# Optimization experiments

Hardware: AMD Instinct MI355X
Metric: run time of the kernel (lower is better)

The kernel has to match this reference:

```python
import jax, jax.numpy as jnp
import numpy as np


def _norm_group(pts, ref):
    # pts: [B,T,N,2], ref: [B,T,1,2]. Subtract reference point, divide both coords
    # by max(width,height) of the relative bbox (per frame), guarding scale==0.
    rel = pts - ref
    w = rel[..., 0].max(axis=-1) - rel[..., 0].min(axis=-1)
    h = rel[..., 1].max(axis=-1) - rel[..., 1].min(axis=-1)
    s = jnp.maximum(w, h)
    s = jnp.where(s == 0, jnp.ones_like(s), s)
    return rel / s[..., None, None]


def _prepare_input(x):
    B, T, _ = x.shape
    pts = x.reshape(B, T, 133, 2)
    left = _norm_group(pts[:, :, 91:112], pts[:, :, 9:10]).reshape(B, T, 42)
    right = _norm_group(pts[:, :, 112:133], pts[:, :, 10:11]).reshape(B, T, 42)
    center = pts[:, :, 0:1]
    left_arm = _norm_group(pts[:, :, (5, 7, 9), :], center).reshape(B, T, 6)
    right_arm = _norm_group(pts[:, :, (6, 8, 10), :], center).reshape(B, T, 6)
    return right, right_arm, left, left_arm


def _lstm(x, wih, whh, bih, bhh):
    # x: [B,T,F]; PyTorch gate order i,f,g,o. Returns all hidden states [B,T,H].
    B = x.shape[0]
    H = whh.shape[1]
    pre = jnp.einsum('btf,gf->btg', x, wih) + bih  # [B,T,4H]
    pre = pre.transpose(1, 0, 2)  # time-major for scan
    h0 = jnp.zeros((B, H), x.dtype)
    c0 = jnp.zeros((B, H), x.dtype)

    def step(carry, xt):
        h, c = carry
        g = xt + h @ whh.T + bhh
        i, f, gg, o = jnp.split(g, 4, axis=-1)
        i = jax.nn.sigmoid(i)
        f = jax.nn.sigmoid(f)
        gg = jnp.tanh(gg)
        o = jax.nn.sigmoid(o)
        c = f * c + i * gg
        h = o * jnp.tanh(c)
        return (h, c), h

    _, hs = jax.lax.scan(step, (h0, c0), pre)
    return hs.transpose(1, 0, 2)


def setup_inputs() -> dict:
    key = jax.random.key(0)
    ks = jax.random.split(key, 24)
    B, T = 128, 512
    NUM_CLASSES = 250
    HID = 2 * 64 + 2 * 32  # 192
    s = 0.1

    def p(k, shape):
        return jax.random.normal(k, shape, dtype=jnp.float32) * s

    inp = {'x': jax.random.normal(ks[0], (B, T, 266), dtype=jnp.float32)}
    # right hand LSTM: 42 -> 64
    inp['wih_rh'] = p(ks[1], (256, 42)); inp['whh_rh'] = p(ks[2], (256, 64))
    inp['bih_rh'] = p(ks[3], (256,));   inp['bhh_rh'] = p(ks[4], (256,))
    # right arm LSTM: 6 -> 32
    inp['wih_ra'] = p(ks[5], (128, 6));  inp['whh_ra'] = p(ks[6], (128, 32))
    inp['bih_ra'] = p(ks[7], (128,));   inp['bhh_ra'] = p(ks[8], (128,))
    # left hand LSTM: 42 -> 64
    inp['wih_lh'] = p(ks[9], (256, 42)); inp['whh_lh'] = p(ks[10], (256, 64))
    inp['bih_lh'] = p(ks[11], (256,));  inp['bhh_lh'] = p(ks[12], (256,))
    # left arm LSTM: 6 -> 32
    inp['wih_la'] = p(ks[13], (128, 6)); inp['whh_la'] = p(ks[14], (128, 32))
    inp['bih_la'] = p(ks[15], (128,));  inp['bhh_la'] = p(ks[16], (128,))
    # attention (Linear(192,1,bias=False)) and fc
    inp['att_w'] = p(ks[17], (1, HID))
    inp['fc_w'] = p(ks[18], (NUM_CLASSES, HID))
    inp['fc_b'] = p(ks[19], (NUM_CLASSES,))
    return inp


def reference(x, wih_rh, whh_rh, bih_rh, bhh_rh,
              wih_ra, whh_ra, bih_ra, bhh_ra,
              wih_lh, whh_lh, bih_lh, bhh_lh,
              wih_la, whh_la, bih_la, bhh_la,
              att_w, fc_w, fc_b):
    rh, ra, lh, la = _prepare_input(x)
    rh_out = _lstm(rh, wih_rh, whh_rh, bih_rh, bhh_rh)
    ra_out = _lstm(ra, wih_ra, whh_ra, bih_ra, bhh_ra)
    lh_out = _lstm(lh, wih_lh, whh_lh, bih_lh, bhh_lh)
    la_out = _lstm(la, wih_la, whh_la, bih_la, bhh_la)
    combined = jnp.concatenate([rh_out, ra_out, lh_out, la_out], axis=2)  # [B,T,192]
    scores = jnp.einsum('bth,oh->bto', combined, att_w)  # [B,T,1]
    weights = jax.nn.softmax(scores, axis=1)
    context = jnp.sum(weights * combined, axis=1)  # [B,192]
    out = context @ fc_w.T + fc_b  # [B,num_classes]
    return out, weights
```

## Files before the change

kernel.cpp:

```cpp
#include <hip/hip_runtime.h>
#include <math.h>

#define BATCH 128
#define TLEN 512
#define XF 266
#define HID 192
#define NC 250

typedef __attribute__((ext_vector_type(8))) short short8;
typedef __attribute__((ext_vector_type(4))) float float4v;

#define NL2E  -1.4426950408889634f
#define NL2E2 -2.8853900817779268f

__device__ __forceinline__ unsigned short f2bf(float f) {
  unsigned u = __float_as_uint(f);
  u += 0x7FFF + ((u >> 16) & 1);
  return (unsigned short)(u >> 16);
}
__device__ __forceinline__ float bf2f(unsigned short s) {
  return __uint_as_float(((unsigned)s) << 16);
}

__device__ __forceinline__ float exp2i(float x) {
#if __has_builtin(__builtin_amdgcn_exp2f)
  return __builtin_amdgcn_exp2f(x);
#else
  float r;
  asm("v_exp_f32 %0, %1" : "=v"(r) : "v"(x));
  return r;
#endif
}

__device__ __forceinline__ void lds_barrier() {
  asm volatile("s_waitcnt lgkmcnt(0)\n\ts_barrier" ::: "memory");
}


__device__ __forceinline__ void norm_hand(const float* __restrict__ xp,
                                          unsigned short* __restrict__ fp,
                                          int p0, int refp, int hs) {
  float rx = xp[2 * refp], ry = xp[2 * refp + 1];
  float px[21], py[21];
  float minx = 1e30f, maxx = -1e30f, miny = 1e30f, maxy = -1e30f;
#pragma unroll
  for (int i = 0; i < 21; ++i) {
    float ax = xp[2 * (p0 + i)] - rx;
    float ay = xp[2 * (p0 + i) + 1] - ry;
    px[i] = ax; py[i] = ay;
    minx = fminf(minx, ax); maxx = fmaxf(maxx, ax);
    miny = fminf(miny, ay); maxy = fmaxf(maxy, ay);
  }
  float s = fmaxf(maxx - minx, maxy - miny);
  if (s == 0.f) s = 1.f;
  float inv = 1.f / s;
#pragma unroll
  for (int i = 0; i < 21; ++i) {
    fp[2 * i] = f2bf(px[i] * inv);
    fp[2 * i + 1] = f2bf(py[i] * inv);
  }
  for (int i = 42; i < hs; ++i) fp[i] = 0;
}

__device__ __forceinline__ void norm_arm(const float* __restrict__ xp,
                                         unsigned short* __restrict__ fp,
                                         int a, int b, int c) {
  float rx = xp[0], ry = xp[1];
  float x0 = xp[2 * a] - rx, y0 = xp[2 * a + 1] - ry;
  float x1 = xp[2 * b] - rx, y1 = xp[2 * b + 1] - ry;
  float x2 = xp[2 * c] - rx, y2 = xp[2 * c + 1] - ry;
  float w = fmaxf(fmaxf(x0, x1), x2) - fminf(fminf(x0, x1), x2);
  float h = fmaxf(fmaxf(y0, y1), y2) - fminf(fminf(y0, y1), y2);
  float s = fmaxf(w, h);
  if (s == 0.f) s = 1.f;
  float inv = 1.f / s;
  fp[0] = f2bf(x0 * inv); fp[1] = f2bf(y0 * inv);
  fp[2] = f2bf(x1 * inv); fp[3] = f2bf(y1 * inv);
  fp[4] = f2bf(x2 * inv); fp[5] = f2bf(y2 * inv);
  fp[6] = 0; fp[7] = 0;
}

__global__ __launch_bounds__(256) void prep_kernel(
    const float* __restrict__ x,
    unsigned short* __restrict__ fHR, unsigned short* __restrict__ fHL,
    unsigned short* __restrict__ fAR, unsigned short* __restrict__ fAL,
    int mode) {
  int idx = blockIdx.x * 256 + threadIdx.x;
  if (idx >= BATCH * TLEN) return;
  int b = idx >> 9, t = idx & 511;
  const float* xp = x + (size_t)idx * XF;
  size_t hoff, aoff;
  int hs;
  if (mode) {
    hs = 64;
    int vh = b & 7;
    int rowh = (vh >> 1) * 4 + (vh & 1);
    hoff = (((size_t)(b >> 3) * TLEN + t) * 16 + rowh) * 64;
    int va = b & 15;
    int rowa = (va >> 3) * 16 + ((va & 7) >> 1) * 4 + (va & 1);
    aoff = (((size_t)(b >> 4) * TLEN + t) * 32 + rowa) * 8;
  } else {
    hs = 48;
    hoff = (((size_t)(b >> 4) * TLEN + t) * 16 + (b & 15)) * 48;
    aoff = (((size_t)(b >> 5) * TLEN + t) * 32 + (b & 31)) * 8;
  }
  norm_hand(xp, fHR + hoff, 112, 10, hs);
  norm_hand(xp, fHL + hoff, 91, 9, hs);
  norm_arm (xp, fAR + aoff, 6, 8, 10);
  norm_arm (xp, fAL + aoff, 5, 7, 9);
}


__global__ __launch_bounds__(256) void pack_kernel(
    int mode,
    const float* __restrict__ wi_rh, const float* __restrict__ wh_rh,
    const float* __restrict__ wi_ra, const float* __restrict__ wh_ra,
    const float* __restrict__ wi_lh, const float* __restrict__ wh_lh,
    const float* __restrict__ wi_la, const float* __restrict__ wh_la,
    unsigned short* __restrict__ btA_r, unsigned short* __restrict__ btA_l,
    unsigned short* __restrict__ btH_r, unsigned short* __restrict__ btH_l,
    unsigned short* __restrict__ btArm_r, unsigned short* __restrict__ btArm_l) {
  int blk = blockIdx.x, tid = threadIdx.x;
  if (blk < 2) {
    const float* wi = blk ? wi_lh : wi_rh;
    const float* wh = blk ? wh_lh : wh_rh;
    unsigned short* dst = blk ? btA_l : btA_r;
    if (mode) {
      for (int i = tid; i < 256 * 64; i += 256) {
        int g = i >> 6, k = i & 63;
        float s = ((g >> 6) == 2) ? NL2E2 : NL2E;
        dst[i] = f2bf(k < 42 ? wi[g * 42 + k] * s : 0.f);
      }
    } else {
      for (int i = tid; i < 256 * 128; i += 256) {
        int g = i >> 7, k = i & 127;
        float s = ((g >> 6) == 2) ? NL2E2 : NL2E;
        float v = (k < 42) ? wi[g * 42 + k] : (k < 64 ? 0.f : wh[g * 64 + (k - 64)]);
        dst[i] = f2bf(v * s);
      }
    }
  } else if (blk < 4) {
    if (mode) {
      const float* wh = (blk == 3) ? wh_lh : wh_rh;
      unsigned short* dst = (blk == 3) ? btH_l : btH_r;
      for (int i = tid; i < 256 * 64; i += 256) {
        int g = i >> 6;
        float s = ((g >> 6) == 2) ? NL2E2 : NL2E;
        dst[i] = f2bf(wh[i] * s);
      }
    }
  } else {
    const float* wi = (blk == 5) ? wi_la : wi_ra;
    const float* wh = (blk == 5) ? wh_la : wh_ra;
    unsigned short* dst = (blk == 5) ? btArm_l : btArm_r;
    for (int i = tid; i < 128 * 64; i += 256) {
      int g = i >> 6, k = i & 63;
      float s = ((g >> 5) == 2) ? NL2E2 : NL2E;
      float v = (k < 6) ? wi[g * 6 + k] : (k < 32 ? 0.f : wh[g * 32 + (k - 32)]);
      dst[i] = f2bf(v * s);
    }
  }
}


__global__ __launch_bounds__(256, 1) void pregemm_kernel(
    const unsigned short* __restrict__ f64R, const unsigned short* __restrict__ f64L,
    const unsigned short* __restrict__ btiR, const unsigned short* __restrict__ btiL,
    const float* __restrict__ biR, const float* __restrict__ bhR,
    const float* __restrict__ biL, const float* __restrict__ bhL,
    unsigned short* __restrict__ preR, unsigned short* __restrict__ preL) {
  int bx = blockIdx.x;
  int lr = bx >> 8, tile = (bx >> 4) & 15, tc = bx & 15;
  const unsigned short* f64 = lr ? f64L : f64R;
  const unsigned short* bti = lr ? btiL : btiR;
  const float* bi = lr ? biL : biR;
  const float* bh = lr ? bhL : bhR;
  unsigned short* pre = lr ? preL : preR;
  int tid = threadIdx.x, lane = tid & 63;
  int q = tid >> 6, n = lane & 15, quad = lane >> 4;
  float sq = (q == 2) ? NL2E2 : NL2E;

  short8 Vb[4][2];
  float bias[4];
#pragma unroll
  for (int jg = 0; jg < 4; ++jg) {
    int g = q * 64 + jg * 16 + n;
    bias[jg] = (bi[g] + bh[g]) * sq;
#pragma unroll
    for (int c = 0; c < 2; ++c)
      Vb[jg][c] = *(const short8*)(bti + (size_t)g * 64 + c * 32 + quad * 8);
  }

  for (int i = 0; i < 32; ++i) {
    int t = tc * 32 + i;
    const unsigned short* ap = f64 + ((size_t)(tile * 512 + t) * 16 + n) * 64 + quad * 8;
    short8 Va0 = *(const short8*)ap;
    short8 Va1 = *(const short8*)(ap + 32);
    unsigned short* pb = pre + (size_t)(tile * 512 + t) * 2048 + n * 32 + quad * 8 + q * 2;
#pragma unroll
    for (int jg = 0; jg < 4; ++jg) {
      float4v acc = {bias[jg], bias[jg], bias[jg], bias[jg]};
      acc = __builtin_amdgcn_mfma_f32_16x16x32_bf16(Va0, Vb[jg][0], acc, 0, 0, 0);
      acc = __builtin_amdgcn_mfma_f32_16x16x32_bf16(Va1, Vb[jg][1], acc, 0, 0, 0);
      unsigned w = (unsigned)f2bf(acc[0]) | ((unsigned)f2bf(acc[1]) << 16);
      *(unsigned*)(pb + (size_t)jg * 512) = w;
    }
  }
}


template <int H, int CH, int STR, int MB, int SCH, int HOFF, bool HOIST, int RV>
__device__ __forceinline__ void lstm_core(
    unsigned short* __restrict__ Ab0, unsigned short* __restrict__ Ab1,
    const unsigned short* __restrict__ Bt,
    const float* __restrict__ bi, const float* __restrict__ bh,
    const unsigned short* __restrict__ featp,
    const unsigned short* __restrict__ prep_,
    unsigned short* __restrict__ combbase,
    int b0, int mrow0, int j0) {
  constexpr int K = CH * 32;
  constexpr int XSH = MB * SCH * 8;
  constexpr int JQ = H / 4;
  constexpr int VR = (RV == 4) ? MB : MB / 2;
  int tid = threadIdx.x;
  int lane = tid & 63, n = lane & 15, quad = lane >> 4;

  short8 Vb[4][CH];
  float bias[4];
#pragma unroll
  for (int q = 0; q < 4; ++q) {
    int g = q * H + j0 + n;
    if (!HOIST) bias[q] = (bi[g] + bh[g]) * ((q == 2) ? NL2E2 : NL2E);
#pragma unroll
    for (int c = 0; c < CH; ++c)
      Vb[q][c] = *(const short8*)(Bt + (size_t)g * K + c * 32 + quad * 8);
  }

  for (int i = tid; i < MB * STR; i += 256) { Ab0[i] = 0; Ab1[i] = 0; }
  __syncthreads();

  bool st = false;
  unsigned short *xd0 = nullptr, *xd1 = nullptr;
  const unsigned short* fp = nullptr;
  short8 xE, xO;
  if (!HOIST) {
    st = tid < MB * SCH;
    int sm = tid / SCH, sc8 = tid % SCH;
    xd0 = Ab0 + sm * STR + sc8 * 8;
    xd1 = Ab1 + sm * STR + sc8 * 8;
    fp = featp + tid * 8;
    if (st) {
      *(short8*)xd0 = *(const short8*)fp;
      xO = *(const short8*)(fp + XSH);
      xE = *(const short8*)(fp + 2 * (size_t)XSH);
    }
    fp += 3 * (size_t)XSH;
  }

  const unsigned short* ppE = nullptr;
  const unsigned short* ppO = nullptr;
  short8 pE, pO;
  if (HOIST) {
    const unsigned short* pp0 = prep_ + (size_t)j0 * 32 + n * 32 + quad * 8;
    pE = *(const short8*)pp0;
    pO = *(const short8*)(pp0 + 2048);
    ppE = pp0 + 2 * (size_t)2048;
    ppO = pp0 + 3 * (size_t)2048;
  }

  float4v cc = {0.f, 0.f, 0.f, 0.f};
  __syncthreads();

  const unsigned short* ard0 = Ab0 + (mrow0 + n) * STR;
  const unsigned short* ard1 = Ab1 + (mrow0 + n) * STR;
  unsigned short* hw0 = Ab0 + (mrow0 + quad * 4) * STR + HOFF + j0 + n;
  unsigned short* hw1 = Ab1 + (mrow0 + quad * 4) * STR + HOFF + j0 + n;

  int vi = tid / JQ, fjq = tid % JQ;
  bool fon = tid < VR * JQ;
  int fm = (RV == 4) ? vi
                     : ((vi >> 3) * 16 + ((vi & 7) >> 1) * 4 + (vi & 1));
  const unsigned short* fl0 = Ab0 + fm * STR + HOFF + fjq * 4;
  const unsigned short* fl1 = Ab1 + fm * STR + HOFF + fjq * 4;
  unsigned short* cfp = combbase + ((size_t)(b0 + vi) * TLEN) * HID + fjq * 4;

#define ACT_AND_WRITE(hw)                                                     \
  _Pragma("unroll")                                                           \
  for (int r = 0; r < RV; ++r) {                                              \
    float Ei = exp2i(acc[0][r]);                                              \
    float Ef = exp2i(acc[1][r]);                                              \
    float Eg = exp2i(acc[2][r]);                                              \
    float Eo = exp2i(acc[3][r]);                                              \
    float gf = __builtin_amdgcn_rcpf(1.f + Ef);                               \
    float ig = (1.f - Eg) * __builtin_amdgcn_rcpf((1.f + Ei) * (1.f + Eg));   \
    float cv = fmaf(gf, cc[r], ig);                                           \
    cc[r] = cv;                                                               \
    float Ec = exp2i(cv * NL2E2);                                             \
    float hv = (1.f - Ec) * __builtin_amdgcn_rcpf((1.f + Eo) * (1.f + Ec));   \
    (hw)[r * STR] = f2bf(hv);                                                 \
  }

  for (int tt = 0; tt < TLEN; tt += 2) {
    {
      const int t = tt;
      if (fon && t > 0) {
        *(uint2*)cfp = *(const uint2*)fl0;
        cfp += HID;
      }
      short8 Va[CH];
#pragma unroll
      for (int c = 0; c < CH; ++c)
        Va[c] = *(const short8*)(ard0 + c * 32 + quad * 8);

      float4v acc[4];
      if (HOIST) {
#pragma unroll
        for (int q = 0; q < 4; ++q) {
          acc[q][0] = bf2f((unsigned short)pE[q * 2]);
          acc[q][1] = bf2f((unsigned short)pE[q * 2 + 1]);
          acc[q][2] = 0.f; acc[q][3] = 0.f;
        }
        if (t + 2 < TLEN) pE = *(const short8*)ppE;
        ppE += 2 * (size_t)2048;
      } else {
#pragma unroll
        for (int q = 0; q < 4; ++q)
          acc[q] = (float4v){bias[q], bias[q], bias[q], bias[q]};
      }
#pragma unroll
      for (int q = 0; q < 4; ++q)
#pragma unroll
        for (int c = 0; c < CH; ++c)
          acc[q] = __builtin_amdgcn_mfma_f32_16x16x32_bf16(Va[c], Vb[q][c], acc[q], 0, 0, 0);

      if (!HOIST) {
        if (st) {
          *(short8*)xd1 = xO;
          if (t + 3 < TLEN) xO = *(const short8*)fp;
        }
        fp += XSH;
      }

      ACT_AND_WRITE(hw1)
      lds_barrier();
    }
    {
      const int t = tt + 1;
      if (fon) {
        *(uint2*)cfp = *(const uint2*)fl1;
        cfp += HID;
      }
      short8 Va[CH];
#pragma unroll
      for (int c = 0; c < CH; ++c)
        Va[c] = *(const short8*)(ard1 + c * 32 + quad * 8);

      float4v acc[4];
      if (HOIST) {
#pragma unroll
        for (int q = 0; q < 4; ++q) {
          acc[q][0] = bf2f((unsigned short)pO[q * 2]);
          acc[q][1] = bf2f((unsigned short)pO[q * 2 + 1]);
          acc[q][2] = 0.f; acc[q][3] = 0.f;
        }
        if (t + 2 < TLEN) pO = *(const short8*)ppO;
        ppO += 2 * (size_t)2048;
      } else {
#pragma unroll
        for (int q = 0; q < 4; ++q)
          acc[q] = (float4v){bias[q], bias[q], bias[q], bias[q]};
      }
#pragma unroll
      for (int q = 0; q < 4; ++q)
#pragma unroll
        for (int c = 0; c < CH; ++c)
          acc[q] = __builtin_amdgcn_mfma_f32_16x16x32_bf16(Va[c], Vb[q][c], acc[q], 0, 0, 0);

      if (!HOIST) {
        if (st) {
          if (t + 1 < TLEN) *(short8*)xd0 = xE;
          if (t + 3 < TLEN) xE = *(const short8*)fp;
        }
        fp += XSH;
      }

      ACT_AND_WRITE(hw0)
      lds_barrier();
    }
  }

  if (fon) *(uint2*)cfp = *(const uint2*)fl0;
#undef ACT_AND_WRITE
}

__global__ __launch_bounds__(256, 1) void lstm_hoist(
    const unsigned short* __restrict__ fAR, const unsigned short* __restrict__ fAL,
    const unsigned short* __restrict__ btH_r, const unsigned short* __restrict__ btH_l,
    const unsigned short* __restrict__ btArm_r, const unsigned short* __restrict__ btArm_l,
    const unsigned short* __restrict__ preR, const unsigned short* __restrict__ preL,
    const float* __restrict__ b1i, const float* __restrict__ b1h,
    const float* __restrict__ b3i, const float* __restrict__ b3h,
    unsigned short* __restrict__ combined) {
  __shared__ __align__(16) unsigned short A0[2304];
  __shared__ __align__(16) unsigned short A1[2304];
  int blk = blockIdx.x;
  int wave = threadIdx.x >> 6;
  if (blk < 32) {
    int lr = blk >> 4, tl = blk & 15;
    lstm_core<64, 2, 72, 16, 0, 0, true, 2>(
        A0, A1, lr ? btH_l : btH_r, nullptr, nullptr, nullptr,
        (lr ? preL : preR) + (size_t)tl * 512 * 2048,
        combined + (lr ? 96 : 0), tl * 8, 0, wave * 16);
  } else {
    int a = blk - 32;
    int la = a >> 3, tl = a & 7;
    lstm_core<32, 2, 72, 32, 1, 32, false, 2>(
        A0, A1, la ? btArm_l : btArm_r, la ? b3i : b1i, la ? b3h : b1h,
        (la ? fAL : fAR) + (size_t)tl * 512 * 256, nullptr,
        combined + (la ? 160 : 64), tl * 16, (wave >> 1) * 16, (wave & 1) * 16);
  }
}

__global__ __launch_bounds__(256, 1) void lstm_fb(
    const unsigned short* __restrict__ fHR, const unsigned short* __restrict__ fHL,
    const unsigned short* __restrict__ fAR, const unsigned short* __restrict__ fAL,
    const unsigned short* __restrict__ btA_r, const unsigned short* __restrict__ btA_l,
    const unsigned short* __restrict__ btArm_r, const unsigned short* __restrict__ btArm_l,
    const float* __restrict__ b0i, const float* __restrict__ b0h,
    const float* __restrict__ b1i, const float* __restrict__ b1h,
    const float* __restrict__ b2i, const float* __restrict__ b2h,
    const float* __restrict__ b3i, const float* __restrict__ b3h,
    unsigned short* __restrict__ combined) {
  __shared__ __align__(16) unsigned short A0[2304];
  __shared__ __align__(16) unsigned short A1[2304];
  int blk = blockIdx.x;
  int wave = threadIdx.x >> 6;
  if (blk < 16) {
    int lr = blk >> 3, tl = blk & 7;
    lstm_core<64, 4, 136, 16, 6, 64, false, 4>(
        A0, A1, lr ? btA_l : btA_r, lr ? b2i : b0i, lr ? b2h : b0h,
        (lr ? fHL : fHR) + (size_t)tl * 512 * 768, nullptr,
        combined + (lr ? 96 : 0), tl * 16, 0, wave * 16);
  } else {
    int a = blk - 16;
    int la = a >> 2, tl = a & 3;
    lstm_core<32, 2, 72, 32, 1, 32, false, 4>(
        A0, A1, la ? btArm_l : btArm_r, la ? b3i : b1i, la ? b3h : b1h,
        (la ? fAL : fAR) + (size_t)tl * 512 * 256, nullptr,
        combined + (la ? 160 : 64), tl * 32, (wave >> 1) * 16, (wave & 1) * 16);
  }
}


__global__ __launch_bounds__(512) void attn_kernel(const unsigned short* __restrict__ combined,
                                                   const float* __restrict__ att_w,
                                                   const float* __restrict__ fc_w,
                                                   const float* __restrict__ fc_b,
                                                   float* __restrict__ dout) {
  __shared__ float sc[TLEN];
  __shared__ float aw[HID];
  __shared__ float pctx[8][HID];
  __shared__ float ctx[HID];
  __shared__ float red[8];
  int b = blockIdx.x, tid = threadIdx.x;
  int lane = tid & 63, wave = tid >> 6;
  const unsigned short* cb = combined + (size_t)b * TLEN * HID;
  if (tid < HID) aw[tid] = att_w[tid];
  __syncthreads();
  float a0 = aw[lane], a1 = aw[lane + 64], a2 = aw[lane + 128];

  int t0 = wave * 64;
  for (int t = t0; t < t0 + 64; t += 2) {
    const unsigned short* r0 = cb + (size_t)t * HID;
    const unsigned short* r1 = r0 + HID;
    float p0 = a0 * bf2f(r0[lane]) + a1 * bf2f(r0[lane + 64]) + a2 * bf2f(r0[lane + 128]);
    float p1 = a0 * bf2f(r1[lane]) + a1 * bf2f(r1[lane + 64]) + a2 * bf2f(r1[lane + 128]);
#pragma unroll
    for (int o = 32; o; o >>= 1) {
      p0 += __shfl_xor(p0, o, 64);
      p1 += __shfl_xor(p1, o, 64);
    }
    if (lane == 0) { sc[t] = p0; sc[t + 1] = p1; }
  }
  __syncthreads();

  float e = sc[tid];
  float lmax = e;
#pragma unroll
  for (int o = 32; o; o >>= 1) lmax = fmaxf(lmax, __shfl_xor(lmax, o, 64));
  if (lane == 0) red[wave] = lmax;
  __syncthreads();
  float m = red[0];
#pragma unroll
  for (int w = 1; w < 8; ++w) m = fmaxf(m, red[w]);
  __syncthreads();
  float ex = __expf(e - m);
  float ls = ex;
#pragma unroll
  for (int o = 32; o; o >>= 1) ls += __shfl_xor(ls, o, 64);
  if (lane == 0) red[wave] = ls;
  __syncthreads();
  float S = red[0];
#pragma unroll
  for (int w = 1; w < 8; ++w) S += red[w];
  float wgt = ex / S;
  sc[tid] = wgt;
  dout[BATCH * NC + b * TLEN + tid] = wgt;
  __syncthreads();

#pragma unroll
  for (int p = 0; p < 3; ++p) {
    int h = p * 64 + lane;
    float c0 = 0.f, c1 = 0.f, c2 = 0.f, c3 = 0.f;
    for (int t = t0; t < t0 + 64; t += 4) {
      c0 += sc[t] * bf2f(cb[(size_t)t * HID + h]);
      c1 += sc[t + 1] * bf2f(cb[(size_t)(t + 1) * HID + h]);
      c2 += sc[t + 2] * bf2f(cb[(size_t)(t + 2) * HID + h]);
      c3 += sc[t + 3] * bf2f(cb[(size_t)(t + 3) * HID + h]);
    }
    pctx[wave][h] = (c0 + c1) + (c2 + c3);
  }
  __syncthreads();
  if (tid < HID) {
    float s = pctx[0][tid];
#pragma unroll
    for (int w = 1; w < 8; ++w) s += pctx[w][tid];
    ctx[tid] = s;
  }
  __syncthreads();

  if (tid < NC) {
    const float* wr = fc_w + (size_t)tid * HID;
    float s0 = fc_b[tid], s1 = 0.f, s2 = 0.f, s3 = 0.f;
#pragma unroll
    for (int h = 0; h < HID; h += 4) {
      s0 += ctx[h] * wr[h];
      s1 += ctx[h + 1] * wr[h + 1];
      s2 += ctx[h + 2] * wr[h + 2];
      s3 += ctx[h + 3] * wr[h + 3];
    }
    dout[b * NC + tid] = (s0 + s1) + (s2 + s3);
  }
}


extern "C" void kernel_launch(void* const* d_in, const int* in_sizes, int n_in,
                              void* d_out, int out_size, void* d_ws, size_t ws_size,
                              hipStream_t stream) {
  const float* x = (const float*)d_in[0];
  const float* wih_rh = (const float*)d_in[1];
  const float* whh_rh = (const float*)d_in[2];
  const float* bih_rh = (const float*)d_in[3];
  const float* bhh_rh = (const float*)d_in[4];
  const float* wih_ra = (const float*)d_in[5];
  const float* whh_ra = (const float*)d_in[6];
  const float* bih_ra = (const float*)d_in[7];
  const float* bhh_ra = (const float*)d_in[8];
  const float* wih_lh = (const float*)d_in[9];
  const float* whh_lh = (const float*)d_in[10];
  const float* bih_lh = (const float*)d_in[11];
  const float* bhh_lh = (const float*)d_in[12];
  const float* wih_la = (const float*)d_in[13];
  const float* whh_la = (const float*)d_in[14];
  const float* bih_la = (const float*)d_in[15];
  const float* bhh_la = (const float*)d_in[16];
  const float* att_w = (const float*)d_in[17];
  const float* fc_w = (const float*)d_in[18];
  const float* fc_b = (const float*)d_in[19];

  const size_t SZ_COMB   = (size_t)BATCH * TLEN * HID * 2;
  const size_t SZ_FARM_H = (size_t)8 * TLEN * 32 * 8 * 2;
  const size_t SZ_FARM_F = (size_t)4 * TLEN * 32 * 8 * 2;
  const size_t SZ_F64    = (size_t)16 * TLEN * 16 * 64 * 2;
  const size_t SZ_F48    = (size_t)8 * TLEN * 16 * 48 * 2;
  const size_t SZ_PRE    = (size_t)16 * TLEN * 2048 * 2;
  const size_t NEED_FULL = SZ_COMB + 2 * SZ_FARM_H + 2 * SZ_F64 + 2 * SZ_PRE +
                           2 * 32768 + 2 * 32768 + 2 * 16384;
  bool hoist = ws_size >= NEED_FULL;

  char* p = (char*)d_ws;
  unsigned short* combined = (unsigned short*)p; p += SZ_COMB;
  unsigned short *fAR, *fAL;
  unsigned short *fHR, *fHL, *preR = nullptr, *preL = nullptr;
  unsigned short *btA_r, *btA_l, *btH_r = nullptr, *btH_l = nullptr, *btArm_r, *btArm_l;
  if (hoist) {
    fAR = (unsigned short*)p; p += SZ_FARM_H;
    fAL = (unsigned short*)p; p += SZ_FARM_H;
    fHR = (unsigned short*)p; p += SZ_F64;
    fHL = (unsigned short*)p; p += SZ_F64;
    preR = (unsigned short*)p; p += SZ_PRE;
    preL = (unsigned short*)p; p += SZ_PRE;
    btA_r = (unsigned short*)p; p += 32768;
    btA_l = (unsigned short*)p; p += 32768;
    btH_r = (unsigned short*)p; p += 32768;
    btH_l = (unsigned short*)p; p += 32768;
  } else {
    fAR = (unsigned short*)p; p += SZ_FARM_F;
    fAL = (unsigned short*)p; p += SZ_FARM_F;
    fHR = (unsigned short*)p; p += SZ_F48;
    fHL = (unsigned short*)p; p += SZ_F48;
    btA_r = (unsigned short*)p; p += 65536;
    btA_l = (unsigned short*)p; p += 65536;
    btH_r = btA_r; btH_l = btA_l;
  }
  btArm_r = (unsigned short*)p; p += 16384;
  btArm_l = (unsigned short*)p;

  prep_kernel<<<dim3((BATCH * TLEN + 255) / 256), 256, 0, stream>>>(
      x, fHR, fHL, fAR, fAL, hoist ? 1 : 0);
  pack_kernel<<<dim3(6), 256, 0, stream>>>(
      hoist ? 1 : 0,
      wih_rh, whh_rh, wih_ra, whh_ra, wih_lh, whh_lh, wih_la, whh_la,
      btA_r, btA_l, btH_r, btH_l, btArm_r, btArm_l);
  if (hoist) {
    pregemm_kernel<<<dim3(512), 256, 0, stream>>>(
        fHR, fHL, btA_r, btA_l, bih_rh, bhh_rh, bih_lh, bhh_lh, preR, preL);
    lstm_hoist<<<dim3(48), 256, 0, stream>>>(
        fAR, fAL, btH_r, btH_l, btArm_r, btArm_l, preR, preL,
        bih_ra, bhh_ra, bih_la, bhh_la, combined);
  } else {
    lstm_fb<<<dim3(24), 256, 0, stream>>>(
        fHR, fHL, fAR, fAL, btA_r, btA_l, btArm_r, btArm_l,
        bih_rh, bhh_rh, bih_ra, bhh_ra, bih_lh, bhh_lh, bih_la, bhh_la, combined);
  }
  attn_kernel<<<dim3(BATCH), 512, 0, stream>>>(combined, att_w, fc_w, fc_b, (float*)d_out);
}
```

Before: 438.8 us.

## Restructure hoisted LSTM into single-wave blocks with 4 sequences each

Replaces the 256-thread recurrent LSTM blocks, which shared hidden state through LDS with a block barrier every timestep, with 128 single-wave blocks that each run 4 batch sequences. Each wave keeps all gate weights in registers and computes every gate tile itself, so the per-step s_barrier goes away and only an LDS wait remains. The input and pre-gate layouts are reorganized to match, and weight packing is folded into the consuming kernels, which removes the pack launch on the hoisted path. The trade-off is more MFMA work per wave and much heavier register use, across more blocks in parallel.

```diff
diff --git a/kernel.cpp b/kernel.cpp
--- a/kernel.cpp
+++ b/kernel.cpp
@@ -30,10 +30,6 @@
   asm("v_exp_f32 %0, %1" : "=v"(r) : "v"(x));
   return r;
 #endif
-}
-
-__device__ __forceinline__ void lds_barrier() {
-  asm volatile("s_waitcnt lgkmcnt(0)\n\ts_barrier" ::: "memory");
 }
 
 
@@ -93,12 +89,8 @@
   int hs;
   if (mode) {
     hs = 64;
-    int vh = b & 7;
-    int rowh = (vh >> 1) * 4 + (vh & 1);
-    hoff = (((size_t)(b >> 3) * TLEN + t) * 16 + rowh) * 64;
-    int va = b & 15;
-    int rowa = (va >> 3) * 16 + ((va & 7) >> 1) * 4 + (va & 1);
-    aoff = (((size_t)(b >> 4) * TLEN + t) * 32 + rowa) * 8;
+    hoff = (((size_t)(b >> 4) * TLEN + t) * 16 + (b & 15)) * 64;
+    aoff = (((size_t)(b >> 2) * TLEN + t) * 4 + (b & 3)) * 8;
   } else {
     hs = 48;
     hoff = (((size_t)(b >> 4) * TLEN + t) * 16 + (b & 15)) * 48;
@@ -112,47 +104,27 @@
 
 
 __global__ __launch_bounds__(256) void pack_kernel(
-    int mode,
     const float* __restrict__ wi_rh, const float* __restrict__ wh_rh,
     const float* __restrict__ wi_ra, const float* __restrict__ wh_ra,
     const float* __restrict__ wi_lh, const float* __restrict__ wh_lh,
     const float* __restrict__ wi_la, const float* __restrict__ wh_la,
     unsigned short* __restrict__ btA_r, unsigned short* __restrict__ btA_l,
-    unsigned short* __restrict__ btH_r, unsigned short* __restrict__ btH_l,
     unsigned short* __restrict__ btArm_r, unsigned short* __restrict__ btArm_l) {
   int blk = blockIdx.x, tid = threadIdx.x;
   if (blk < 2) {
     const float* wi = blk ? wi_lh : wi_rh;
     const float* wh = blk ? wh_lh : wh_rh;
     unsigned short* dst = blk ? btA_l : btA_r;
-    if (mode) {
-      for (int i = tid; i < 256 * 64; i += 256) {
-        int g = i >> 6, k = i & 63;
-        float s = ((g >> 6) == 2) ? NL2E2 : NL2E;
-        dst[i] = f2bf(k < 42 ? wi[g * 42 + k] * s : 0.f);
-      }
-    } else {
-      for (int i = tid; i < 256 * 128; i += 256) {
-        int g = i >> 7, k = i & 127;
-        float s = ((g >> 6) == 2) ? NL2E2 : NL2E;
-        float v = (k < 42) ? wi[g * 42 + k] : (k < 64 ? 0.f : wh[g * 64 + (k - 64)]);
-        dst[i] = f2bf(v * s);
-      }
-    }
-  } else if (blk < 4) {
-    if (mode) {
-      const float* wh = (blk == 3) ? wh_lh : wh_rh;
-      unsigned short* dst = (blk == 3) ? btH_l : btH_r;
-      for (int i = tid; i < 256 * 64; i += 256) {
-        int g = i >> 6;
-        float s = ((g >> 6) == 2) ? NL2E2 : NL2E;
-        dst[i] = f2bf(wh[i] * s);
-      }
+    for (int i = tid; i < 256 * 128; i += 256) {
+      int g = i >> 7, k = i & 127;
+      float s = ((g >> 6) == 2) ? NL2E2 : NL2E;
+      float v = (k < 42) ? wi[g * 42 + k] : (k < 64 ? 0.f : wh[g * 64 + (k - 64)]);
+      dst[i] = f2bf(v * s);
     }
   } else {
-    const float* wi = (blk == 5) ? wi_la : wi_ra;
-    const float* wh = (blk == 5) ? wh_la : wh_ra;
-    unsigned short* dst = (blk == 5) ? btArm_l : btArm_r;
+    const float* wi = (blk == 3) ? wi_la : wi_ra;
+    const float* wh = (blk == 3) ? wh_la : wh_ra;
+    unsigned short* dst = (blk == 3) ? btArm_l : btArm_r;
     for (int i = tid; i < 128 * 64; i += 256) {
       int g = i >> 6, k = i & 63;
       float s = ((g >> 5) == 2) ? NL2E2 : NL2E;
@@ -165,14 +137,14 @@
 
 __global__ __launch_bounds__(256, 1) void pregemm_kernel(
     const unsigned short* __restrict__ f64R, const unsigned short* __restrict__ f64L,
-    const unsigned short* __restrict__ btiR, const unsigned short* __restrict__ btiL,
+    const float* __restrict__ wiR, const float* __restrict__ wiL,
     const float* __restrict__ biR, const float* __restrict__ bhR,
     const float* __restrict__ biL, const float* __restrict__ bhL,
     unsigned short* __restrict__ preR, unsigned short* __restrict__ preL) {
   int bx = blockIdx.x;
-  int lr = bx >> 8, tile = (bx >> 4) & 15, tc = bx & 15;
+  int lr = bx >> 7, tile = (bx >> 4) & 7, tc = bx & 15;
   const unsigned short* f64 = lr ? f64L : f64R;
-  const unsigned short* bti = lr ? btiL : btiR;
+  const float* wi = lr ? wiL : wiR;
   const float* bi = lr ? biL : biR;
   const float* bh = lr ? bhL : bhR;
   unsigned short* pre = lr ? preL : preR;
@@ -187,8 +159,15 @@
     int g = q * 64 + jg * 16 + n;
     bias[jg] = (bi[g] + bh[g]) * sq;
 #pragma unroll
-    for (int c = 0; c < 2; ++c)
-      Vb[jg][c] = *(const short8*)(bti + (size_t)g * 64 + c * 32 + quad * 8);
+    for (int c = 0; c < 2; ++c) {
+      short8 vb;
+#pragma unroll
+      for (int s = 0; s < 8; ++s) {
+        int k = c * 32 + quad * 8 + s;
+        vb[s] = (short)f2bf(k < 42 ? wi[g * 42 + k] * sq : 0.f);
+      }
+      Vb[jg][c] = vb;
+    }
   }
 
   for (int i = 0; i < 32; ++i) {
@@ -196,32 +175,234 @@
     const unsigned short* ap = f64 + ((size_t)(tile * 512 + t) * 16 + n) * 64 + quad * 8;
     short8 Va0 = *(const short8*)ap;
     short8 Va1 = *(const short8*)(ap + 32);
-    unsigned short* pb = pre + (size_t)(tile * 512 + t) * 2048 + n * 32 + quad * 8 + q * 2;
+    float4v acc[4];
 #pragma unroll
     for (int jg = 0; jg < 4; ++jg) {
-      float4v acc = {bias[jg], bias[jg], bias[jg], bias[jg]};
-      acc = __builtin_amdgcn_mfma_f32_16x16x32_bf16(Va0, Vb[jg][0], acc, 0, 0, 0);
-      acc = __builtin_amdgcn_mfma_f32_16x16x32_bf16(Va1, Vb[jg][1], acc, 0, 0, 0);
-      unsigned w = (unsigned)f2bf(acc[0]) | ((unsigned)f2bf(acc[1]) << 16);
-      *(unsigned*)(pb + (size_t)jg * 512) = w;
-    }
-  }
-}
-
-
-template <int H, int CH, int STR, int MB, int SCH, int HOFF, bool HOIST, int RV>
-__device__ __forceinline__ void lstm_core(
+      acc[jg] = (float4v){bias[jg], bias[jg], bias[jg], bias[jg]};
+      acc[jg] = __builtin_amdgcn_mfma_f32_16x16x32_bf16(Va0, Vb[jg][0], acc[jg], 0, 0, 0);
+      acc[jg] = __builtin_amdgcn_mfma_f32_16x16x32_bf16(Va1, Vb[jg][1], acc[jg], 0, 0, 0);
+    }
+    unsigned short* pb = pre + ((size_t)(tile * 4 + quad) * 512 + t) * 1024 + q * 256 + n * 4;
+#pragma unroll
+    for (int r = 0; r < 4; ++r) {
+      uint2 u;
+      u.x = (unsigned)f2bf(acc[0][r]) | ((unsigned)f2bf(acc[1][r]) << 16);
+      u.y = (unsigned)f2bf(acc[2][r]) | ((unsigned)f2bf(acc[3][r]) << 16);
+      *(uint2*)(pb + r * 64) = u;
+    }
+  }
+}
+
+
+__global__ __launch_bounds__(64, 1) void lstm_hoist(
+    const unsigned short* __restrict__ fAR, const unsigned short* __restrict__ fAL,
+    const float* __restrict__ whh_rh, const float* __restrict__ whh_lh,
+    const float* __restrict__ wih_ra, const float* __restrict__ whh_ra,
+    const float* __restrict__ wih_la, const float* __restrict__ whh_la,
+    const unsigned short* __restrict__ preR, const unsigned short* __restrict__ preL,
+    const float* __restrict__ b1i, const float* __restrict__ b1h,
+    const float* __restrict__ b3i, const float* __restrict__ b3h,
+    unsigned short* __restrict__ combined) {
+  __shared__ __align__(16) unsigned short A[320];
+  int blk = blockIdx.x;
+  int lane = threadIdx.x, n = lane & 15, quad = lane >> 4;
+
+  for (int i = lane; i < 320; i += 64) A[i] = 0;
+  asm volatile("s_waitcnt lgkmcnt(0)" ::: "memory");
+
+  bool rd = (n & 3) == 0;
+  const unsigned short* ar = A + (n >> 2) * 80 + quad * 8;
+
+  if (blk < 64) {
+    int lr = blk >> 5, inst = blk & 31;
+    const float* wq = lr ? whh_lh : whh_rh;
+    const unsigned short* pp = (lr ? preL : preR) +
+        (size_t)inst * 512 * 1024 + quad * 64 + n * 4;
+    unsigned short* cgp = combined +
+        ((size_t)(inst * 4 + quad) * TLEN) * HID + (lr ? 96 : 0) + n;
+
+    short8 Vb[16][2];
+#pragma unroll
+    for (int jt = 0; jt < 16; ++jt) {
+      float sq = ((jt >> 2) == 2) ? NL2E2 : NL2E;
+      int g = jt * 16 + n;
+#pragma unroll
+      for (int c = 0; c < 2; ++c) {
+        short8 vb;
+#pragma unroll
+        for (int s = 0; s < 8; ++s)
+          vb[s] = (short)f2bf(wq[(size_t)g * 64 + c * 32 + quad * 8 + s] * sq);
+        Vb[jt][c] = vb;
+      }
+    }
+    float4v acc[16];
+#pragma unroll
+    for (int jt = 0; jt < 16; ++jt) acc[jt] = (float4v){0.f, 0.f, 0.f, 0.f};
+
+    uint2 pE[4], pO[4];
+#pragma unroll
+    for (int q2 = 0; q2 < 4; ++q2) {
+      pE[q2] = *(const uint2*)(pp + q2 * 256);
+      pO[q2] = *(const uint2*)(pp + 1024 + q2 * 256);
+    }
+    const unsigned short* ppE = pp + 2 * 1024;
+    const unsigned short* ppO = pp + 3 * 1024;
+
+    float cc[4] = {0.f, 0.f, 0.f, 0.f};
+    unsigned short* hw = A + quad * 80 + n;
+
+#define HSTEP(PREG, PPTR, GUARD)                                              \
+    {                                                                         \
+      short8 Va0 = {0, 0, 0, 0, 0, 0, 0, 0};                                  \
+      short8 Va1 = {0, 0, 0, 0, 0, 0, 0, 0};                                  \
+      if (rd) { Va0 = *(const short8*)ar; Va1 = *(const short8*)(ar + 32); }  \
+      _Pragma("unroll")                                                       \
+      for (int q2 = 0; q2 < 4; ++q2) {                                        \
+        acc[q2 * 4 + 0][0] = __uint_as_float(PREG[q2].x << 16);               \
+        acc[q2 * 4 + 1][0] = __uint_as_float(PREG[q2].x & 0xffff0000u);       \
+        acc[q2 * 4 + 2][0] = __uint_as_float(PREG[q2].y << 16);               \
+        acc[q2 * 4 + 3][0] = __uint_as_float(PREG[q2].y & 0xffff0000u);       \
+      }                                                                       \
+      if (GUARD) {                                                            \
+        _Pragma("unroll")                                                     \
+        for (int q2 = 0; q2 < 4; ++q2)                                        \
+          PREG[q2] = *(const uint2*)(PPTR + q2 * 256);                        \
+      }                                                                       \
+      PPTR += 2048;                                                           \
+      _Pragma("unroll")                                                       \
+      for (int jt = 0; jt < 16; ++jt) {                                       \
+        acc[jt] = __builtin_amdgcn_mfma_f32_16x16x32_bf16(Va0, Vb[jt][0], acc[jt], 0, 0, 0); \
+        acc[jt] = __builtin_amdgcn_mfma_f32_16x16x32_bf16(Va1, Vb[jt][1], acc[jt], 0, 0, 0); \
+      }                                                                       \
+      _Pragma("unroll")                                                       \
+      for (int m = 0; m < 4; ++m) {                                           \
+        float Ei = exp2i(acc[m][0]);                                          \
+        float Ef = exp2i(acc[4 + m][0]);                                      \
+        float Eg = exp2i(acc[8 + m][0]);                                      \
+        float Eo = exp2i(acc[12 + m][0]);                                     \
+        float gf = __builtin_amdgcn_rcpf(1.f + Ef);                           \
+        float ig = (1.f - Eg) * __builtin_amdgcn_rcpf((1.f + Ei) * (1.f + Eg)); \
+        float cv = fmaf(gf, cc[m], ig);                                       \
+        cc[m] = cv;                                                           \
+        float Ec = exp2i(cv * NL2E2);                                         \
+        float hv = (1.f - Ec) * __builtin_amdgcn_rcpf((1.f + Eo) * (1.f + Ec)); \
+        unsigned short hb = f2bf(hv);                                         \
+        hw[16 * m] = hb;                                                      \
+        cgp[16 * m] = hb;                                                     \
+      }                                                                       \
+      cgp += HID;                                                             \
+    }
+
+    for (int tt = 0; tt < TLEN; tt += 2) {
+      HSTEP(pE, ppE, (tt + 2 < TLEN))
+      HSTEP(pO, ppO, (tt + 3 < TLEN))
+    }
+#undef HSTEP
+  } else {
+    int a = blk - 64, la = a >> 5, inst = a & 31;
+    const float* wx = la ? wih_la : wih_ra;
+    const float* wh2 = la ? whh_la : whh_ra;
+    const float* bip = la ? b3i : b1i;
+    const float* bhp = la ? b3h : b1h;
+    const unsigned short* fA = (la ? fAL : fAR);
+    unsigned short* cgp = combined +
+        ((size_t)(inst * 4 + quad) * TLEN) * HID + (la ? 160 : 64) + n;
+
+    short8 Vb[8][2];
+    float bias[8];
+#pragma unroll
+    for (int jt = 0; jt < 8; ++jt) {
+      float sq = ((jt >> 1) == 2) ? NL2E2 : NL2E;
+      int g = jt * 16 + n;
+      bias[jt] = (bip[g] + bhp[g]) * sq;
+#pragma unroll
+      for (int c = 0; c < 2; ++c) {
+        short8 vb;
+#pragma unroll
+        for (int s = 0; s < 8; ++s) {
+          int k = c * 32 + quad * 8 + s;
+          float v = (k < 6) ? wx[g * 6 + k] : (k >= 32 ? wh2[g * 32 + (k - 32)] : 0.f);
+          vb[s] = (short)f2bf(v * sq);
+        }
+        Vb[jt][c] = vb;
+      }
+    }
+    float4v acc[8];
+#pragma unroll
+    for (int jt = 0; jt < 8; ++jt) acc[jt] = (float4v){0.f, 0.f, 0.f, 0.f};
+
+    bool stg = (lane >= 48 && lane < 52);
+    const unsigned short* fpp = fA + (size_t)inst * 512 * 32 + (lane - 48) * 8;
+    unsigned short* xdst = A + (lane - 48) * 80;
+    short8 xO, xE;
+    if (stg) {
+      *(short8*)xdst = *(const short8*)fpp;
+      xO = *(const short8*)(fpp + 32);
+      xE = *(const short8*)(fpp + 64);
+    }
+    const unsigned short* fq = fpp + 96;
+    asm volatile("s_waitcnt lgkmcnt(0)" ::: "memory");
+
+    float cc[2] = {0.f, 0.f};
+    unsigned short* hw = A + quad * 80 + 32 + n;
+
+#define ASTEP(XREG, WGUARD, LGUARD)                                           \
+    {                                                                         \
+      short8 Va0 = {0, 0, 0, 0, 0, 0, 0, 0};                                  \
+      short8 Va1 = {0, 0, 0, 0, 0, 0, 0, 0};                                  \
+      if (rd) { Va0 = *(const short8*)ar; Va1 = *(const short8*)(ar + 32); }  \
+      _Pragma("unroll")                                                       \
+      for (int jt = 0; jt < 8; ++jt) acc[jt][0] = bias[jt];                   \
+      _Pragma("unroll")                                                       \
+      for (int jt = 0; jt < 8; ++jt) {                                        \
+        acc[jt] = __builtin_amdgcn_mfma_f32_16x16x32_bf16(Va0, Vb[jt][0], acc[jt], 0, 0, 0); \
+        acc[jt] = __builtin_amdgcn_mfma_f32_16x16x32_bf16(Va1, Vb[jt][1], acc[jt], 0, 0, 0); \
+      }                                                                       \
+      if (stg) {                                                              \
+        if (WGUARD) *(short8*)xdst = XREG;                                    \
+        if (LGUARD) XREG = *(const short8*)fq;                                \
+      }                                                                       \
+      fq += 32;                                                               \
+      _Pragma("unroll")                                                       \
+      for (int m = 0; m < 2; ++m) {                                           \
+        float Ei = exp2i(acc[m][0]);                                          \
+        float Ef = exp2i(acc[2 + m][0]);                                      \
+        float Eg = exp2i(acc[4 + m][0]);                                      \
+        float Eo = exp2i(acc[6 + m][0]);                                      \
+        float gf = __builtin_amdgcn_rcpf(1.f + Ef);                           \
+        float ig = (1.f - Eg) * __builtin_amdgcn_rcpf((1.f + Ei) * (1.f + Eg)); \
+        float cv = fmaf(gf, cc[m], ig);                                       \
+        cc[m] = cv;                                                           \
+        float Ec = exp2i(cv * NL2E2);                                         \
+        float hv = (1.f - Ec) * __builtin_amdgcn_rcpf((1.f + Eo) * (1.f + Ec)); \
+        unsigned short hb = f2bf(hv);                                         \
+        hw[16 * m] = hb;                                                      \
+        cgp[16 * m] = hb;                                                     \
+      }                                                                       \
+      cgp += HID;                                                             \
+    }
+
+    for (int tt = 0; tt < TLEN; tt += 2) {
+      ASTEP(xO, true, (tt + 3 < TLEN))
+      ASTEP(xE, (tt + 2 < TLEN), (tt + 4 < TLEN))
+    }
+#undef ASTEP
+  }
+}
+
+
+template <int H, int CH, int STR, int MB, int SCH, int HOFF, int RV>
+__device__ __forceinline__ void lstm_core_fb(
     unsigned short* __restrict__ Ab0, unsigned short* __restrict__ Ab1,
     const unsigned short* __restrict__ Bt,
     const float* __restrict__ bi, const float* __restrict__ bh,
     const unsigned short* __restrict__ featp,
-    const unsigned short* __restrict__ prep_,
     unsigned short* __restrict__ combbase,
     int b0, int mrow0, int j0) {
   constexpr int K = CH * 32;
   constexpr int XSH = MB * SCH * 8;
   constexpr int JQ = H / 4;
-  constexpr int VR = (RV == 4) ? MB : MB / 2;
+  constexpr int VR = MB;
   int tid = threadIdx.x;
   int lane = tid & 63, n = lane & 15, quad = lane >> 4;
 
@@ -230,7 +411,7 @@
 #pragma unroll
   for (int q = 0; q < 4; ++q) {
     int g = q * H + j0 + n;
-    if (!HOIST) bias[q] = (bi[g] + bh[g]) * ((q == 2) ? NL2E2 : NL2E);
+    bias[q] = (bi[g] + bh[g]) * ((q == 2) ? NL2E2 : NL2E);
 #pragma unroll
     for (int c = 0; c < CH; ++c)
       Vb[q][c] = *(const short8*)(Bt + (size_t)g * K + c * 32 + quad * 8);
@@ -239,34 +420,18 @@
   for (int i = tid; i < MB * STR; i += 256) { Ab0[i] = 0; Ab1[i] = 0; }
   __syncthreads();
 
-  bool st = false;
-  unsigned short *xd0 = nullptr, *xd1 = nullptr;
-  const unsigned short* fp = nullptr;
+  bool st = tid < MB * SCH;
+  int sm = SCH ? tid / SCH : 0, sc8 = SCH ? tid % SCH : 0;
+  unsigned short* xd0 = Ab0 + sm * STR + sc8 * 8;
+  unsigned short* xd1 = Ab1 + sm * STR + sc8 * 8;
+  const unsigned short* fp = featp + tid * 8;
   short8 xE, xO;
-  if (!HOIST) {
-    st = tid < MB * SCH;
-    int sm = tid / SCH, sc8 = tid % SCH;
-    xd0 = Ab0 + sm * STR + sc8 * 8;
-    xd1 = Ab1 + sm * STR + sc8 * 8;
-    fp = featp + tid * 8;
-    if (st) {
-      *(short8*)xd0 = *(const short8*)fp;
-      xO = *(const short8*)(fp + XSH);
-      xE = *(const short8*)(fp + 2 * (size_t)XSH);
-    }
-    fp += 3 * (size_t)XSH;
-  }
-
-  const unsigned short* ppE = nullptr;
-  const unsigned short* ppO = nullptr;
-  short8 pE, pO;
-  if (HOIST) {
-    const unsigned short* pp0 = prep_ + (size_t)j0 * 32 + n * 32 + quad * 8;
-    pE = *(const short8*)pp0;
-    pO = *(const short8*)(pp0 + 2048);
-    ppE = pp0 + 2 * (size_t)2048;
-    ppO = pp0 + 3 * (size_t)2048;
-  }
+  if (st) {
+    *(short8*)xd0 = *(const short8*)fp;
+    xO = *(const short8*)(fp + XSH);
+    xE = *(const short8*)(fp + 2 * (size_t)XSH);
+  }
+  fp += 3 * (size_t)XSH;
 
   float4v cc = {0.f, 0.f, 0.f, 0.f};
   __syncthreads();
@@ -278,13 +443,12 @@
 
   int vi = tid / JQ, fjq = tid % JQ;
   bool fon = tid < VR * JQ;
-  int fm = (RV == 4) ? vi
-                     : ((vi >> 3) * 16 + ((vi & 7) >> 1) * 4 + (vi & 1));
+  int fm = vi;
   const unsigned short* fl0 = Ab0 + fm * STR + HOFF + fjq * 4;
   const unsigned short* fl1 = Ab1 + fm * STR + HOFF + fjq * 4;
   unsigned short* cfp = combbase + ((size_t)(b0 + vi) * TLEN) * HID + fjq * 4;
 
-#define ACT_AND_WRITE(hw)                                                     \
+#define ACT_FB(hw)                                                            \
   _Pragma("unroll")                                                           \
   for (int r = 0; r < RV; ++r) {                                              \
     float Ei = exp2i(acc[0][r]);                                              \
@@ -311,38 +475,22 @@
 #pragma unroll
       for (int c = 0; c < CH; ++c)
         Va[c] = *(const short8*)(ard0 + c * 32 + quad * 8);
-
       float4v acc[4];
-      if (HOIST) {
-#pragma unroll
-        for (int q = 0; q < 4; ++q) {
-          acc[q][0] = bf2f((unsigned short)pE[q * 2]);
-          acc[q][1] = bf2f((unsigned short)pE[q * 2 + 1]);
-          acc[q][2] = 0.f; acc[q][3] = 0.f;
-        }
-        if (t + 2 < TLEN) pE = *(const short8*)ppE;
-        ppE += 2 * (size_t)2048;
-      } else {
-#pragma unroll
-        for (int q = 0; q < 4; ++q)
-          acc[q] = (float4v){bias[q], bias[q], bias[q], bias[q]};
-      }
+#pragma unroll
+      for (int q = 0; q < 4; ++q)
+        acc[q] = (float4v){bias[q], bias[q], bias[q], bias[q]};
 #pragma unroll
       for (int q = 0; q < 4; ++q)
 #pragma unroll
         for (int c = 0; c < CH; ++c)
           acc[q] = __builtin_amdgcn_mfma_f32_16x16x32_bf16(Va[c], Vb[q][c], acc[q], 0, 0, 0);
-
-      if (!HOIST) {
-        if (st) {
-          *(short8*)xd1 = xO;
-          if (t + 3 < TLEN) xO = *(const short8*)fp;
-        }
-        fp += XSH;
+      if (st) {
+        *(short8*)xd1 = xO;
+        if (t + 3 < TLEN) xO = *(const short8*)fp;
       }
-
-      ACT_AND_WRITE(hw1)
-      lds_barrier();
+      fp += XSH;
+      ACT_FB(hw1)
+      asm volatile("s_waitcnt lgkmcnt(0)\n\ts_barrier" ::: "memory");
     }
     {
       const int t = tt + 1;
@@ -354,71 +502,26 @@
 #pragma unroll
       for (int c = 0; c < CH; ++c)
         Va[c] = *(const short8*)(ard1 + c * 32 + quad * 8);
-
       float4v acc[4];
-      if (HOIST) {
-#pragma unroll
-        for (int q = 0; q < 4; ++q) {
-          acc[q][0] = bf2f((unsigned short)pO[q * 2]);
-          acc[q][1] = bf2f((unsigned short)pO[q * 2 + 1]);
-          acc[q][2] = 0.f; acc[q][3] = 0.f;
-        }
-        if (t + 2 < TLEN) pO = *(const short8*)ppO;
-        ppO += 2 * (size_t)2048;
-      } else {
-#pragma unroll
-        for (int q = 0; q < 4; ++q)
-          acc[q] = (float4v){bias[q], bias[q], bias[q], bias[q]};
-      }
+#pragma unroll
+      for (int q = 0; q < 4; ++q)
+        acc[q] = (float4v){bias[q], bias[q], bias[q], bias[q]};
 #pragma unroll
       for (int q = 0; q < 4; ++q)
 #pragma unroll
         for (int c = 0; c < CH; ++c)
           acc[q] = __builtin_amdgcn_mfma_f32_16x16x32_bf16(Va[c], Vb[q][c], acc[q], 0, 0, 0);
-
-      if (!HOIST) {
-        if (st) {
-          if (t + 1 < TLEN) *(short8*)xd0 = xE;
-          if (t + 3 < TLEN) xE = *(const short8*)fp;
-        }
-        fp += XSH;
+      if (st) {
+        if (t + 1 < TLEN) *(short8*)xd0 = xE;
+        if (t + 3 < TLEN) xE = *(const short8*)fp;
       }
-
-      ACT_AND_WRITE(hw0)
-      lds_barrier();
-    }
-  }
-
+      fp += XSH;
+      ACT_FB(hw0)
+      asm volatile("s_waitcnt lgkmcnt(0)\n\ts_barrier" ::: "memory");
+    }
+  }
   if (fon) *(uint2*)cfp = *(const uint2*)fl0;
-#undef ACT_AND_WRITE
-}
-
-__global__ __launch_bounds__(256, 1) void lstm_hoist(
-    const unsigned short* __restrict__ fAR, const unsigned short* __restrict__ fAL,
-    const unsigned short* __restrict__ btH_r, const unsigned short* __restrict__ btH_l,
-    const unsigned short* __restrict__ btArm_r, const unsigned short* __restrict__ btArm_l,
-    const unsigned short* __restrict__ preR, const unsigned short* __restrict__ preL,
-    const float* __restrict__ b1i, const float* __restrict__ b1h,
-    const float* __restrict__ b3i, const float* __restrict__ b3h,
-    unsigned short* __restrict__ combined) {
-  __shared__ __align__(16) unsigned short A0[2304];
-  __shared__ __align__(16) unsigned short A1[2304];
-  int blk = blockIdx.x;
-  int wave = threadIdx.x >> 6;
-  if (blk < 32) {
-    int lr = blk >> 4, tl = blk & 15;
-    lstm_core<64, 2, 72, 16, 0, 0, true, 2>(
-        A0, A1, lr ? btH_l : btH_r, nullptr, nullptr, nullptr,
-        (lr ? preL : preR) + (size_t)tl * 512 * 2048,
-        combined + (lr ? 96 : 0), tl * 8, 0, wave * 16);
-  } else {
-    int a = blk - 32;
-    int la = a >> 3, tl = a & 7;
-    lstm_core<32, 2, 72, 32, 1, 32, false, 2>(
-        A0, A1, la ? btArm_l : btArm_r, la ? b3i : b1i, la ? b3h : b1h,
-        (la ? fAL : fAR) + (size_t)tl * 512 * 256, nullptr,
-        combined + (la ? 160 : 64), tl * 16, (wave >> 1) * 16, (wave & 1) * 16);
-  }
+#undef ACT_FB
 }
 
 __global__ __launch_bounds__(256, 1) void lstm_fb(
@@ -437,16 +540,16 @@
   int wave = threadIdx.x >> 6;
   if (blk < 16) {
     int lr = blk >> 3, tl = blk & 7;
-    lstm_core<64, 4, 136, 16, 6, 64, false, 4>(
+    lstm_core_fb<64, 4, 136, 16, 6, 64, 4>(
         A0, A1, lr ? btA_l : btA_r, lr ? b2i : b0i, lr ? b2h : b0h,
-        (lr ? fHL : fHR) + (size_t)tl * 512 * 768, nullptr,
+        (lr ? fHL : fHR) + (size_t)tl * 512 * 768,
         combined + (lr ? 96 : 0), tl * 16, 0, wave * 16);
   } else {
     int a = blk - 16;
     int la = a >> 2, tl = a & 3;
-    lstm_core<32, 2, 72, 32, 1, 32, false, 4>(
+    lstm_core_fb<32, 2, 72, 32, 1, 32, 4>(
         A0, A1, la ? btArm_l : btArm_r, la ? b3i : b1i, la ? b3h : b1h,
-        (la ? fAL : fAR) + (size_t)tl * 512 * 256, nullptr,
+        (la ? fAL : fAR) + (size_t)tl * 512 * 256,
         combined + (la ? 160 : 64), tl * 32, (wave >> 1) * 16, (wave & 1) * 16);
   }
 }
@@ -569,20 +672,19 @@
   const float* fc_b = (const float*)d_in[19];
 
   const size_t SZ_COMB   = (size_t)BATCH * TLEN * HID * 2;
-  const size_t SZ_FARM_H = (size_t)8 * TLEN * 32 * 8 * 2;
+  const size_t SZ_FARM_H = (size_t)32 * TLEN * 4 * 8 * 2;
   const size_t SZ_FARM_F = (size_t)4 * TLEN * 32 * 8 * 2;
-  const size_t SZ_F64    = (size_t)16 * TLEN * 16 * 64 * 2;
+  const size_t SZ_F64    = (size_t)8 * TLEN * 16 * 64 * 2;
   const size_t SZ_F48    = (size_t)8 * TLEN * 16 * 48 * 2;
-  const size_t SZ_PRE    = (size_t)16 * TLEN * 2048 * 2;
-  const size_t NEED_FULL = SZ_COMB + 2 * SZ_FARM_H + 2 * SZ_F64 + 2 * SZ_PRE +
-                           2 * 32768 + 2 * 32768 + 2 * 16384;
+  const size_t SZ_PRE    = (size_t)32 * TLEN * 1024 * 2;
+  const size_t NEED_FULL = SZ_COMB + 2 * SZ_FARM_H + 2 * SZ_F64 + 2 * SZ_PRE;
   bool hoist = ws_size >= NEED_FULL;
 
   char* p = (char*)d_ws;
   unsigned short* combined = (unsigned short*)p; p += SZ_COMB;
   unsigned short *fAR, *fAL;
   unsigned short *fHR, *fHL, *preR = nullptr, *preL = nullptr;
-  unsigned short *btA_r, *btA_l, *btH_r = nullptr, *btH_l = nullptr, *btArm_r, *btArm_l;
+  unsigned short *btA_r = nullptr, *btA_l = nullptr, *btArm_r = nullptr, *btArm_l = nullptr;
   if (hoist) {
     fAR = (unsigned short*)p; p += SZ_FARM_H;
     fAL = (unsigned short*)p; p += SZ_FARM_H;
@@ -590,10 +692,6 @@
     fHL = (unsigned short*)p; p += SZ_F64;
     preR = (unsigned short*)p; p += SZ_PRE;
     preL = (unsigned short*)p; p += SZ_PRE;
-    btA_r = (unsigned short*)p; p += 32768;
-    btA_l = (unsigned short*)p; p += 32768;
-    btH_r = (unsigned short*)p; p += 32768;
-    btH_l = (unsigned short*)p; p += 32768;
   } else {
     fAR = (unsigned short*)p; p += SZ_FARM_F;
     fAL = (unsigned short*)p; p += SZ_FARM_F;
@@ -601,24 +699,22 @@
     fHL = (unsigned short*)p; p += SZ_F48;
     btA_r = (unsigned short*)p; p += 65536;
     btA_l = (unsigned short*)p; p += 65536;
-    btH_r = btA_r; btH_l = btA_l;
-  }
-  btArm_r = (unsigned short*)p; p += 16384;
-  btArm_l = (unsigned short*)p;
+    btArm_r = (unsigned short*)p; p += 16384;
+    btArm_l = (unsigned short*)p;
+  }
 
   prep_kernel<<<dim3((BATCH * TLEN + 255) / 256), 256, 0, stream>>>(
       x, fHR, fHL, fAR, fAL, hoist ? 1 : 0);
-  pack_kernel<<<dim3(6), 256, 0, stream>>>(
-      hoist ? 1 : 0,
-      wih_rh, whh_rh, wih_ra, whh_ra, wih_lh, whh_lh, wih_la, whh_la,
-      btA_r, btA_l, btH_r, btH_l, btArm_r, btArm_l);
   if (hoist) {
-    pregemm_kernel<<<dim3(512), 256, 0, stream>>>(
-        fHR, fHL, btA_r, btA_l, bih_rh, bhh_rh, bih_lh, bhh_lh, preR, preL);
-    lstm_hoist<<<dim3(48), 256, 0, stream>>>(
-        fAR, fAL, btH_r, btH_l, btArm_r, btArm_l, preR, preL,
-        bih_ra, bhh_ra, bih_la, bhh_la, combined);
+    pregemm_kernel<<<dim3(256), 256, 0, stream>>>(
+        fHR, fHL, wih_rh, wih_lh, bih_rh, bhh_rh, bih_lh, bhh_lh, preR, preL);
+    lstm_hoist<<<dim3(128), 64, 0, stream>>>(
+        fAR, fAL, whh_rh, whh_lh, wih_ra, whh_ra, wih_la, whh_la,
+        preR, preL, bih_ra, bhh_ra, bih_la, bhh_la, combined);
   } else {
+    pack_kernel<<<dim3(4), 256, 0, stream>>>(
+        wih_rh, whh_rh, wih_ra, whh_ra, wih_lh, whh_lh, wih_la, whh_la,
+        btA_r, btA_l, btArm_r, btArm_l);
     lstm_fb<<<dim3(24), 256, 0, stream>>>(
         fHR, fHL, fAR, fAL, btA_r, btA_l, btArm_r, btArm_l,
         bih_rh, bhh_rh, bih_ra, bhh_ra, bih_lh, bhh_lh, bih_la, bhh_la, combined);
```

Measured after the change: 572.5 us. 30.5% more time.
